# Kernel tuning notes

Hardware: AMD Instinct MI355X
Metric: run time of the kernel (lower is better)

Reference implementation:

```python
import jax, jax.numpy as jnp
import numpy as np

NH, NKVH, HD = 32, 8, 128
SCALE = 0.08838834764831845  # 1/sqrt(128)
SEQ, CTX = 1024, 3072       # new chunk tokens, cached context tokens
NSLOTS = 8192               # e.g. 512 blocks * block_size 16, slot-flattened


def setup_inputs() -> dict:
    key = jax.random.key(0)
    ks = jax.random.split(key, 5)
    q = jax.random.normal(ks[0], (SEQ, NH * HD), dtype=jnp.float32)
    k = jax.random.normal(ks[1], (SEQ, NKVH * HD), dtype=jnp.float32)
    v = jax.random.normal(ks[2], (SEQ, NKVH * HD), dtype=jnp.float32)
    k_cache = jax.random.normal(ks[3], (NSLOTS, NKVH, HD), dtype=jnp.float32)
    v_cache = jax.random.normal(ks[4], (NSLOTS, NKVH, HD), dtype=jnp.float32)
    # new chunk is stored right after the context region
    slot_mapping = jnp.arange(SEQ, dtype=jnp.int32) + CTX
    context_slots = jnp.arange(CTX, dtype=jnp.int32)
    return {"q": q, "k": k, "v": v, "k_cache": k_cache, "v_cache": v_cache,
            "slot_mapping": slot_mapping, "context_slots": context_slots}


def reference(q, k, v, k_cache, v_cache, slot_mapping, context_slots):
    seq = q.shape[0]
    ctx = context_slots.shape[0]
    qh = q.reshape(seq, NH, HD)
    kh = k.reshape(seq, NKVH, HD)
    vh = v.reshape(seq, NKVH, HD)

    # store_kv_cache: scatter new chunk k/v into paged cache slots
    kc = k_cache.at[slot_mapping].set(kh)
    vc = v_cache.at[slot_mapping].set(vh)

    # gather cached context, then chunked-prefill attention over [ctx | chunk]
    k_all = jnp.concatenate([kc[context_slots], kh], axis=0)  # [L, nkvh, hd]
    v_all = jnp.concatenate([vc[context_slots], vh], axis=0)  # [L, nkvh, hd]
    L = ctx + seq

    group = NH // NKVH
    qg = qh.reshape(seq, NKVH, group, HD) * SCALE
    scores = jnp.einsum('qkgd,lkd->kgql', qg, k_all)  # [nkvh, group, seq, L]

    # full visibility of cached context, causal within the new chunk
    mask = jnp.arange(L)[None, :] <= (ctx + jnp.arange(seq))[:, None]  # [seq, L]
    scores = jnp.where(mask[None, None], scores, jnp.finfo(scores.dtype).min)
    p = jax.nn.softmax(scores, axis=-1)

    o = jnp.einsum('kgql,lkd->qkgd', p, v_all)  # [seq, nkvh, group, hd]
    return o.reshape(seq, NH * HD)
```

## Files before the change

kernel.cpp:

```cpp
#include <hip/hip_runtime.h>

#define NH 32
#define NKVH 8
#define HD 128
#define GRP 4
#define SCALE 0.08838834764831845f

typedef __attribute__((ext_vector_type(8))) __bf16 bf16x8;
typedef __attribute__((ext_vector_type(4))) float f32x4;
typedef __attribute__((ext_vector_type(8))) unsigned short ushort8;

__device__ inline unsigned short f2bf(float x) {
  unsigned int u = __float_as_uint(x);
  u += 0x7fffu + ((u >> 16) & 1u);
  return (unsigned short)(u >> 16);
}

__device__ inline float dpp_max16(float x) {
  x = fmaxf(x, __int_as_float(__builtin_amdgcn_mov_dpp(__float_as_int(x), 0xB1, 0xF, 0xF, true)));
  x = fmaxf(x, __int_as_float(__builtin_amdgcn_mov_dpp(__float_as_int(x), 0x4E, 0xF, 0xF, true)));
  x = fmaxf(x, __int_as_float(__builtin_amdgcn_mov_dpp(__float_as_int(x), 0x141, 0xF, 0xF, true)));
  x = fmaxf(x, __int_as_float(__builtin_amdgcn_mov_dpp(__float_as_int(x), 0x140, 0xF, 0xF, true)));
  return x;
}
__device__ inline float dpp_sum16(float x) {
  x += __int_as_float(__builtin_amdgcn_mov_dpp(__float_as_int(x), 0xB1, 0xF, 0xF, true));
  x += __int_as_float(__builtin_amdgcn_mov_dpp(__float_as_int(x), 0x4E, 0xF, 0xF, true));
  x += __int_as_float(__builtin_amdgcn_mov_dpp(__float_as_int(x), 0x141, 0xF, 0xF, true));
  x += __int_as_float(__builtin_amdgcn_mov_dpp(__float_as_int(x), 0x140, 0xF, 0xF, true));
  return x;
}

__device__ inline void load_lds16(const unsigned short* g, unsigned short* l) {
  __builtin_amdgcn_global_load_lds((const __attribute__((address_space(1))) unsigned int*)g,
                                   (__attribute__((address_space(3))) unsigned int*)l, 16, 0, 0);
}

#define PSTR 72

__global__ __launch_bounds__(256) void prepass_kernel(
    const float* __restrict__ k, const float* __restrict__ v,
    const float* __restrict__ kc, const float* __restrict__ vc,
    const int* __restrict__ slots,
    unsigned short* __restrict__ Kws, unsigned short* __restrict__ Vws,
    int ctx, int L, int kblocks)
{
  if (blockIdx.x < (unsigned)kblocks) {
    const int idx = blockIdx.x * 256 + threadIdx.x;
    const int L8  = L * 8;
    const int kvh = idx / L8;
    const int r2  = idx - kvh * L8;
    const int l   = r2 >> 3;
    const int c16 = idx & 7;
    const float* src = (l < ctx)
        ? kc + ((size_t)slots[l] * NKVH + kvh) * HD + c16 * 16
        : k + (size_t)(l - ctx) * (NKVH * HD) + kvh * HD + c16 * 16;
    float4 f[4];
#pragma unroll
    for (int i = 0; i < 4; ++i) f[i] = ((const float4*)src)[i];
    unsigned short* tile = Kws + (size_t)kvh * L * HD + (size_t)(l >> 6) * 8192;
    const int r = l & 63;
    const int c0 = (2 * c16) ^ (r & 7);
    const int c1 = (2 * c16 + 1) ^ (r & 7);
    ushort8 w0, w1;
    w0[0]=f2bf(f[0].x); w0[1]=f2bf(f[0].y); w0[2]=f2bf(f[0].z); w0[3]=f2bf(f[0].w);
    w0[4]=f2bf(f[1].x); w0[5]=f2bf(f[1].y); w0[6]=f2bf(f[1].z); w0[7]=f2bf(f[1].w);
    w1[0]=f2bf(f[2].x); w1[1]=f2bf(f[2].y); w1[2]=f2bf(f[2].z); w1[3]=f2bf(f[2].w);
    w1[4]=f2bf(f[3].x); w1[5]=f2bf(f[3].y); w1[6]=f2bf(f[3].z); w1[7]=f2bf(f[3].w);
    *(ushort8*)&tile[r * 128 + c0 * 8] = w0;
    *(ushort8*)&tile[r * 128 + c1 * 8] = w1;
  } else {
    const int idx = (blockIdx.x - kblocks) * 256 + threadIdx.x;
    const int d   = idx & 127;
    const int t2  = idx >> 7;
    const int L16 = L >> 4;
    const int kvh = t2 / L16;
    const int lc  = t2 - kvh * L16;
    const int l0  = lc * 16;
    unsigned short vals[16];
#pragma unroll
    for (int i = 0; i < 16; ++i) {
      const int l = l0 + i;
      const float* sp = (l < ctx)
          ? vc + ((size_t)slots[l] * NKVH + kvh) * HD + d
          : v + (size_t)(l - ctx) * (NKVH * HD) + kvh * HD + d;
      vals[i] = f2bf(*sp);
    }
    unsigned short* tile = Vws + (size_t)kvh * L * HD + (size_t)(l0 >> 6) * 8192;
    const int lt  = l0 & 63;
    const int cl0 = lt >> 3;
    ushort8 w0, w1;
#pragma unroll
    for (int i = 0; i < 8; ++i) { w0[i] = vals[i]; w1[i] = vals[8 + i]; }
    *(ushort8*)&tile[d * 64 + ((cl0 ^ (d & 7)) * 8)] = w0;
    *(ushort8*)&tile[d * 64 + (((cl0 + 1) ^ (d & 7)) * 8)] = w1;
  }
}

__global__ __launch_bounds__(256, 2) void attn_kernel(
    const float* __restrict__ q,
    const unsigned short* __restrict__ Kws, const unsigned short* __restrict__ Vws,
    float* __restrict__ out, int ctx, int L)
{
  __shared__ __align__(16) unsigned short Ks[2][8192];
  __shared__ __align__(16) unsigned short VTs[2][8192];
  __shared__ __align__(16) unsigned short Ps[4 * 16 * PSTR];

  const int bx   = blockIdx.x;
  const int kvh  = bx & 7;
  const int g    = (bx >> 3) & 3;
  const int qb   = bx >> 5;
  const int q0   = qb * 64;
  const int head = kvh * GRP + g;

  const int tid  = threadIdx.x;
  const int wave = tid >> 6;
  const int lane = tid & 63;
  const int col  = lane & 15;
  const int quad = lane >> 4;

  bf16x8 qf[4];
  {
    const float* qp = q + (size_t)(q0 + wave * 16 + col) * (NH * HD) + head * HD;
#pragma unroll
    for (int kt = 0; kt < 4; ++kt) {
      const float4 a = *(const float4*)(qp + kt * 32 + quad * 8);
      const float4 b = *(const float4*)(qp + kt * 32 + quad * 8 + 4);
      union { ushort8 u; bf16x8 h; } w;
      w.u[0]=f2bf(a.x*SCALE); w.u[1]=f2bf(a.y*SCALE); w.u[2]=f2bf(a.z*SCALE); w.u[3]=f2bf(a.w*SCALE);
      w.u[4]=f2bf(b.x*SCALE); w.u[5]=f2bf(b.y*SCALE); w.u[6]=f2bf(b.z*SCALE); w.u[7]=f2bf(b.w*SCALE);
      qf[kt] = w.h;
    }
  }

  f32x4 accO[8];
#pragma unroll
  for (int i = 0; i < 8; ++i) accO[i] = (f32x4){0.f, 0.f, 0.f, 0.f};
  float mrow[4] = {-1e30f, -1e30f, -1e30f, -1e30f};
  float lrow[4] = {0.f, 0.f, 0.f, 0.f};

  const int rowbase = q0 + wave * 16 + quad * 4;
  const size_t kvbase = (size_t)kvh * L * HD;
  const int n_tiles = (ctx + q0 + 64) >> 6;

  auto dma_tile = [&](int t, int b) {
    const unsigned short* kg = Kws + kvbase + (size_t)t * 8192;
    const unsigned short* vg = Vws + kvbase + (size_t)t * 8192;
#pragma unroll
    for (int j = 0; j < 4; ++j) {
      const int ch = wave * 4 + j;
      load_lds16(kg + ch * 512 + lane * 8, &Ks[b][ch * 512]);
      load_lds16(vg + ch * 512 + lane * 8, &VTs[b][ch * 512]);
    }
  };

  dma_tile(0, 0);

  for (int it = 0; it < n_tiles; ++it) {
    __syncthreads();

    if (it + 1 < n_tiles) dma_tile(it + 1, (it + 1) & 1);

    const unsigned short* Kb = Ks[it & 1];
    const unsigned short* Vb = VTs[it & 1];
    const int kb = it << 6;

    f32x4 S[4];
#pragma unroll
    for (int nt = 0; nt < 4; ++nt) S[nt] = (f32x4){0.f, 0.f, 0.f, 0.f};
#pragma unroll
    for (int kt = 0; kt < 4; ++kt)
#pragma unroll
      for (int nt = 0; nt < 4; ++nt) {
        const int row = nt * 16 + col;
        const bf16x8 kf = *(const bf16x8*)&Kb[row * 128 + (((kt * 4 + quad) ^ (row & 7)) << 3)];
        S[nt] = __builtin_amdgcn_mfma_f32_16x16x32_bf16(qf[kt], kf, S[nt], 0, 0, 0);
      }

    if (kb + 63 > ctx + q0 + wave * 16) {
#pragma unroll
      for (int r = 0; r < 4; ++r) {
        const int bound = ctx + rowbase + r;
#pragma unroll
        for (int nt = 0; nt < 4; ++nt) {
          const int l = kb + nt * 16 + col;
          if (l > bound) S[nt][r] = -1e30f;
        }
      }
    }

    float alpha[4];
#pragma unroll
    for (int r = 0; r < 4; ++r) {
      float mx = fmaxf(fmaxf(S[0][r], S[1][r]), fmaxf(S[2][r], S[3][r]));
      mx = dpp_max16(mx);
      const float mnew = fmaxf(mrow[r], mx);
      alpha[r] = __expf(mrow[r] - mnew);
      float rs = 0.f;
#pragma unroll
      for (int nt = 0; nt < 4; ++nt) {
        const float p = __expf(S[nt][r] - mnew);
        S[nt][r] = p;
        rs += p;
      }
      rs = dpp_sum16(rs);
      lrow[r] = lrow[r] * alpha[r] + rs;
      mrow[r] = mnew;
    }
#pragma unroll
    for (int dd = 0; dd < 8; ++dd)
#pragma unroll
      for (int r = 0; r < 4; ++r)
        accO[dd][r] *= alpha[r];

    unsigned short* pw = &Ps[wave * 16 * PSTR];
#pragma unroll
    for (int nt = 0; nt < 4; ++nt)
#pragma unroll
      for (int r = 0; r < 4; ++r)
        pw[(quad * 4 + r) * PSTR + nt * 16 + col] = f2bf(S[nt][r]);
    asm volatile("s_waitcnt lgkmcnt(0)" ::: "memory");

    bf16x8 pf[2];
    pf[0] = *(const bf16x8*)&pw[col * PSTR + quad * 8];
    pf[1] = *(const bf16x8*)&pw[col * PSTR + 32 + quad * 8];

#pragma unroll
    for (int nt = 0; nt < 8; ++nt)
#pragma unroll
      for (int kt = 0; kt < 2; ++kt) {
        const int d = nt * 16 + col;
        const bf16x8 vf = *(const bf16x8*)&Vb[d * 64 + (((kt * 4 + quad) ^ (d & 7)) << 3)];
        accO[nt] = __builtin_amdgcn_mfma_f32_16x16x32_bf16(pf[kt], vf, accO[nt], 0, 0, 0);
      }
  }

  float inv[4];
#pragma unroll
  for (int r = 0; r < 4; ++r) inv[r] = 1.0f / lrow[r];
  float* op = out + head * HD;
#pragma unroll
  for (int r = 0; r < 4; ++r) {
    float* orow = op + (size_t)(rowbase + r) * (NH * HD);
#pragma unroll
    for (int nt = 0; nt < 8; ++nt)
      orow[nt * 16 + col] = accO[nt][r] * inv[r];
  }
}

extern "C" void kernel_launch(void* const* d_in, const int* in_sizes, int n_in,
                              void* d_out, int out_size, void* d_ws, size_t ws_size,
                              hipStream_t stream) {
  const float* q  = (const float*)d_in[0];
  const float* k  = (const float*)d_in[1];
  const float* v  = (const float*)d_in[2];
  const float* kc = (const float*)d_in[3];
  const float* vc = (const float*)d_in[4];
  const int* ctx_slots = (const int*)d_in[6];
  float* out = (float*)d_out;

  const int seq = in_sizes[0] / (NH * HD);
  const int ctx = in_sizes[6];
  const int L   = ctx + seq;

  unsigned short* Kws = (unsigned short*)d_ws;
  unsigned short* Vws = Kws + (size_t)NKVH * L * HD;

  const int kthreads = NKVH * L * (HD / 16);
  const int vthreads = NKVH * (L / 16) * HD;
  const int kblocks  = kthreads / 256;
  const int vblocks  = vthreads / 256;
  prepass_kernel<<<kblocks + vblocks, 256, 0, stream>>>(k, v, kc, vc, ctx_slots,
                                                        Kws, Vws, ctx, L, kblocks);

  const int nblocks = (seq / 64) * GRP * NKVH;
  attn_kernel<<<nblocks, 256, 0, stream>>>(q, Kws, Vws, out, ctx, L);
}
```

Baseline: 246.4 us.

## Split K/V prepass and give each attention wave two query row tiles

The fused prepass is split into a K conversion kernel and a V kernel that transposes a 64-row tile through shared memory, so global V reads become coalesced float4 loads instead of strided scalar loads. The attention kernel now runs 2 waves per block, each handling 32 query rows. Each K/V fragment read from LDS therefore feeds two MFMAs, halving LDS traffic per FLOP. The cost is higher register pressure and fewer waves per block, which may reduce latency hiding.

```diff
diff --git a/kernel.cpp b/kernel.cpp
--- a/kernel.cpp
+++ b/kernel.cpp
@@ -38,73 +38,79 @@
 
 #define PSTR 72
 
-__global__ __launch_bounds__(256) void prepass_kernel(
-    const float* __restrict__ k, const float* __restrict__ v,
-    const float* __restrict__ kc, const float* __restrict__ vc,
-    const int* __restrict__ slots,
-    unsigned short* __restrict__ Kws, unsigned short* __restrict__ Vws,
-    int ctx, int L, int kblocks)
+__global__ __launch_bounds__(256) void kprep(
+    const float* __restrict__ k, const float* __restrict__ kc,
+    const int* __restrict__ slots, unsigned short* __restrict__ Kws, int ctx, int L)
 {
-  if (blockIdx.x < (unsigned)kblocks) {
-    const int idx = blockIdx.x * 256 + threadIdx.x;
-    const int L8  = L * 8;
-    const int kvh = idx / L8;
-    const int r2  = idx - kvh * L8;
-    const int l   = r2 >> 3;
-    const int c16 = idx & 7;
-    const float* src = (l < ctx)
-        ? kc + ((size_t)slots[l] * NKVH + kvh) * HD + c16 * 16
-        : k + (size_t)(l - ctx) * (NKVH * HD) + kvh * HD + c16 * 16;
-    float4 f[4];
-#pragma unroll
-    for (int i = 0; i < 4; ++i) f[i] = ((const float4*)src)[i];
-    unsigned short* tile = Kws + (size_t)kvh * L * HD + (size_t)(l >> 6) * 8192;
-    const int r = l & 63;
-    const int c0 = (2 * c16) ^ (r & 7);
-    const int c1 = (2 * c16 + 1) ^ (r & 7);
-    ushort8 w0, w1;
-    w0[0]=f2bf(f[0].x); w0[1]=f2bf(f[0].y); w0[2]=f2bf(f[0].z); w0[3]=f2bf(f[0].w);
-    w0[4]=f2bf(f[1].x); w0[5]=f2bf(f[1].y); w0[6]=f2bf(f[1].z); w0[7]=f2bf(f[1].w);
-    w1[0]=f2bf(f[2].x); w1[1]=f2bf(f[2].y); w1[2]=f2bf(f[2].z); w1[3]=f2bf(f[2].w);
-    w1[4]=f2bf(f[3].x); w1[5]=f2bf(f[3].y); w1[6]=f2bf(f[3].z); w1[7]=f2bf(f[3].w);
-    *(ushort8*)&tile[r * 128 + c0 * 8] = w0;
-    *(ushort8*)&tile[r * 128 + c1 * 8] = w1;
-  } else {
-    const int idx = (blockIdx.x - kblocks) * 256 + threadIdx.x;
-    const int d   = idx & 127;
-    const int t2  = idx >> 7;
-    const int L16 = L >> 4;
-    const int kvh = t2 / L16;
-    const int lc  = t2 - kvh * L16;
-    const int l0  = lc * 16;
-    unsigned short vals[16];
-#pragma unroll
-    for (int i = 0; i < 16; ++i) {
-      const int l = l0 + i;
-      const float* sp = (l < ctx)
-          ? vc + ((size_t)slots[l] * NKVH + kvh) * HD + d
-          : v + (size_t)(l - ctx) * (NKVH * HD) + kvh * HD + d;
-      vals[i] = f2bf(*sp);
-    }
-    unsigned short* tile = Vws + (size_t)kvh * L * HD + (size_t)(l0 >> 6) * 8192;
-    const int lt  = l0 & 63;
-    const int cl0 = lt >> 3;
-    ushort8 w0, w1;
-#pragma unroll
-    for (int i = 0; i < 8; ++i) { w0[i] = vals[i]; w1[i] = vals[8 + i]; }
-    *(ushort8*)&tile[d * 64 + ((cl0 ^ (d & 7)) * 8)] = w0;
-    *(ushort8*)&tile[d * 64 + (((cl0 + 1) ^ (d & 7)) * 8)] = w1;
+  const int idx = blockIdx.x * 256 + threadIdx.x;
+  const int L8  = L * 8;
+  const int kvh = idx / L8;
+  const int r2  = idx - kvh * L8;
+  const int l   = r2 >> 3;
+  const int c16 = idx & 7;
+  const float* src = (l < ctx)
+      ? kc + ((size_t)slots[l] * NKVH + kvh) * HD + c16 * 16
+      : k + (size_t)(l - ctx) * (NKVH * HD) + kvh * HD + c16 * 16;
+  float4 f[4];
+#pragma unroll
+  for (int i = 0; i < 4; ++i) f[i] = ((const float4*)src)[i];
+  unsigned short* tile = Kws + (size_t)kvh * L * HD + (size_t)(l >> 6) * 8192;
+  const int r  = l & 63;
+  const int c0 = (2 * c16) ^ (r & 7);
+  const int c1 = (2 * c16 + 1) ^ (r & 7);
+  ushort8 w0, w1;
+  w0[0]=f2bf(f[0].x); w0[1]=f2bf(f[0].y); w0[2]=f2bf(f[0].z); w0[3]=f2bf(f[0].w);
+  w0[4]=f2bf(f[1].x); w0[5]=f2bf(f[1].y); w0[6]=f2bf(f[1].z); w0[7]=f2bf(f[1].w);
+  w1[0]=f2bf(f[2].x); w1[1]=f2bf(f[2].y); w1[2]=f2bf(f[2].z); w1[3]=f2bf(f[2].w);
+  w1[4]=f2bf(f[3].x); w1[5]=f2bf(f[3].y); w1[6]=f2bf(f[3].z); w1[7]=f2bf(f[3].w);
+  *(ushort8*)&tile[r * 128 + c0 * 8] = w0;
+  *(ushort8*)&tile[r * 128 + c1 * 8] = w1;
+}
+
+__global__ __launch_bounds__(256) void vprep(
+    const float* __restrict__ v, const float* __restrict__ vc,
+    const int* __restrict__ slots, unsigned short* __restrict__ Vws,
+    int ctx, int L, int ntiles)
+{
+  __shared__ __align__(16) unsigned short VT[8192];
+  const int t   = blockIdx.x % ntiles;
+  const int kvh = blockIdx.x / ntiles;
+  const int tid = threadIdx.x;
+  const int l   = tid >> 2;
+  const int ds  = tid & 3;
+  const int lg  = t * 64 + l;
+  const float* sp = (lg < ctx)
+      ? vc + ((size_t)slots[lg] * NKVH + kvh) * HD
+      : v + (size_t)(lg - ctx) * (NKVH * HD) + kvh * HD;
+  sp += ds * 32;
+  float4 f[8];
+#pragma unroll
+  for (int i = 0; i < 8; ++i) f[i] = ((const float4*)sp)[i];
+  const int c  = l >> 3;
+  const int lo = l & 7;
+#pragma unroll
+  for (int i = 0; i < 8; ++i) {
+    const int d0 = ds * 32 + i * 4;
+    VT[(d0+0)*64 + ((c ^ ((d0+0)&7)) << 3) + lo] = f2bf(f[i].x);
+    VT[(d0+1)*64 + ((c ^ ((d0+1)&7)) << 3) + lo] = f2bf(f[i].y);
+    VT[(d0+2)*64 + ((c ^ ((d0+2)&7)) << 3) + lo] = f2bf(f[i].z);
+    VT[(d0+3)*64 + ((c ^ ((d0+3)&7)) << 3) + lo] = f2bf(f[i].w);
   }
-}
-
-__global__ __launch_bounds__(256, 2) void attn_kernel(
+  __syncthreads();
+  ushort8* dst = (ushort8*)(Vws + (size_t)kvh * L * HD + (size_t)t * 8192);
+  const ushort8* s8 = (const ushort8*)VT;
+#pragma unroll
+  for (int i = 0; i < 4; ++i) dst[i * 256 + tid] = s8[i * 256 + tid];
+}
+
+__global__ __launch_bounds__(128, 1) void attn_kernel(
     const float* __restrict__ q,
     const unsigned short* __restrict__ Kws, const unsigned short* __restrict__ Vws,
     float* __restrict__ out, int ctx, int L)
 {
   __shared__ __align__(16) unsigned short Ks[2][8192];
   __shared__ __align__(16) unsigned short VTs[2][8192];
-  __shared__ __align__(16) unsigned short Ps[4 * 16 * PSTR];
+  __shared__ __align__(16) unsigned short Ps[2 * 32 * PSTR];
 
   const int bx   = blockIdx.x;
   const int kvh  = bx & 7;
@@ -119,9 +125,10 @@
   const int col  = lane & 15;
   const int quad = lane >> 4;
 
-  bf16x8 qf[4];
-  {
-    const float* qp = q + (size_t)(q0 + wave * 16 + col) * (NH * HD) + head * HD;
+  bf16x8 qf[2][4];
+#pragma unroll
+  for (int mt = 0; mt < 2; ++mt) {
+    const float* qp = q + (size_t)(q0 + wave * 32 + mt * 16 + col) * (NH * HD) + head * HD;
 #pragma unroll
     for (int kt = 0; kt < 4; ++kt) {
       const float4 a = *(const float4*)(qp + kt * 32 + quad * 8);
@@ -129,17 +136,21 @@
       union { ushort8 u; bf16x8 h; } w;
       w.u[0]=f2bf(a.x*SCALE); w.u[1]=f2bf(a.y*SCALE); w.u[2]=f2bf(a.z*SCALE); w.u[3]=f2bf(a.w*SCALE);
       w.u[4]=f2bf(b.x*SCALE); w.u[5]=f2bf(b.y*SCALE); w.u[6]=f2bf(b.z*SCALE); w.u[7]=f2bf(b.w*SCALE);
-      qf[kt] = w.h;
+      qf[mt][kt] = w.h;
     }
   }
 
-  f32x4 accO[8];
-#pragma unroll
-  for (int i = 0; i < 8; ++i) accO[i] = (f32x4){0.f, 0.f, 0.f, 0.f};
-  float mrow[4] = {-1e30f, -1e30f, -1e30f, -1e30f};
-  float lrow[4] = {0.f, 0.f, 0.f, 0.f};
-
-  const int rowbase = q0 + wave * 16 + quad * 4;
+  f32x4 accO[2][8];
+#pragma unroll
+  for (int mt = 0; mt < 2; ++mt)
+#pragma unroll
+    for (int i = 0; i < 8; ++i) accO[mt][i] = (f32x4){0.f, 0.f, 0.f, 0.f};
+  float mrow[2][4], lrow[2][4];
+#pragma unroll
+  for (int mt = 0; mt < 2; ++mt)
+#pragma unroll
+    for (int r = 0; r < 4; ++r) { mrow[mt][r] = -1e30f; lrow[mt][r] = 0.f; }
+
   const size_t kvbase = (size_t)kvh * L * HD;
   const int n_tiles = (ctx + q0 + 64) >> 6;
 
@@ -147,8 +158,8 @@
     const unsigned short* kg = Kws + kvbase + (size_t)t * 8192;
     const unsigned short* vg = Vws + kvbase + (size_t)t * 8192;
 #pragma unroll
-    for (int j = 0; j < 4; ++j) {
-      const int ch = wave * 4 + j;
+    for (int j = 0; j < 8; ++j) {
+      const int ch = wave * 8 + j;
       load_lds16(kg + ch * 512 + lane * 8, &Ks[b][ch * 512]);
       load_lds16(vg + ch * 512 + lane * 8, &VTs[b][ch * 512]);
     }
@@ -165,65 +176,80 @@
     const unsigned short* Vb = VTs[it & 1];
     const int kb = it << 6;
 
-    f32x4 S[4];
-#pragma unroll
-    for (int nt = 0; nt < 4; ++nt) S[nt] = (f32x4){0.f, 0.f, 0.f, 0.f};
+    f32x4 S[2][4];
+#pragma unroll
+    for (int mt = 0; mt < 2; ++mt)
+#pragma unroll
+      for (int nt = 0; nt < 4; ++nt) S[mt][nt] = (f32x4){0.f, 0.f, 0.f, 0.f};
 #pragma unroll
     for (int kt = 0; kt < 4; ++kt)
 #pragma unroll
       for (int nt = 0; nt < 4; ++nt) {
         const int row = nt * 16 + col;
         const bf16x8 kf = *(const bf16x8*)&Kb[row * 128 + (((kt * 4 + quad) ^ (row & 7)) << 3)];
-        S[nt] = __builtin_amdgcn_mfma_f32_16x16x32_bf16(qf[kt], kf, S[nt], 0, 0, 0);
+        S[0][nt] = __builtin_amdgcn_mfma_f32_16x16x32_bf16(qf[0][kt], kf, S[0][nt], 0, 0, 0);
+        S[1][nt] = __builtin_amdgcn_mfma_f32_16x16x32_bf16(qf[1][kt], kf, S[1][nt], 0, 0, 0);
       }
 
-    if (kb + 63 > ctx + q0 + wave * 16) {
-#pragma unroll
-      for (int r = 0; r < 4; ++r) {
-        const int bound = ctx + rowbase + r;
-#pragma unroll
-        for (int nt = 0; nt < 4; ++nt) {
-          const int l = kb + nt * 16 + col;
-          if (l > bound) S[nt][r] = -1e30f;
+    if (kb + 63 > ctx + q0 + wave * 32) {
+#pragma unroll
+      for (int mt = 0; mt < 2; ++mt) {
+        const int rb = q0 + wave * 32 + mt * 16 + quad * 4;
+#pragma unroll
+        for (int r = 0; r < 4; ++r) {
+          const int bound = ctx + rb + r;
+#pragma unroll
+          for (int nt = 0; nt < 4; ++nt) {
+            const int l = kb + nt * 16 + col;
+            if (l > bound) S[mt][nt][r] = -1e30f;
+          }
         }
       }
     }
 
-    float alpha[4];
-#pragma unroll
-    for (int r = 0; r < 4; ++r) {
-      float mx = fmaxf(fmaxf(S[0][r], S[1][r]), fmaxf(S[2][r], S[3][r]));
-      mx = dpp_max16(mx);
-      const float mnew = fmaxf(mrow[r], mx);
-      alpha[r] = __expf(mrow[r] - mnew);
-      float rs = 0.f;
-#pragma unroll
-      for (int nt = 0; nt < 4; ++nt) {
-        const float p = __expf(S[nt][r] - mnew);
-        S[nt][r] = p;
-        rs += p;
+#pragma unroll
+    for (int mt = 0; mt < 2; ++mt) {
+      float alpha[4];
+#pragma unroll
+      for (int r = 0; r < 4; ++r) {
+        float mx = fmaxf(fmaxf(S[mt][0][r], S[mt][1][r]), fmaxf(S[mt][2][r], S[mt][3][r]));
+        mx = dpp_max16(mx);
+        const float mnew = fmaxf(mrow[mt][r], mx);
+        alpha[r] = __expf(mrow[mt][r] - mnew);
+        float rs = 0.f;
+#pragma unroll
+        for (int nt = 0; nt < 4; ++nt) {
+          const float p = __expf(S[mt][nt][r] - mnew);
+          S[mt][nt][r] = p;
+          rs += p;
+        }
+        rs = dpp_sum16(rs);
+        lrow[mt][r] = lrow[mt][r] * alpha[r] + rs;
+        mrow[mt][r] = mnew;
       }
-      rs = dpp_sum16(rs);
-      lrow[r] = lrow[r] * alpha[r] + rs;
-      mrow[r] = mnew;
-    }
-#pragma unroll
-    for (int dd = 0; dd < 8; ++dd)
-#pragma unroll
-      for (int r = 0; r < 4; ++r)
-        accO[dd][r] *= alpha[r];
-
-    unsigned short* pw = &Ps[wave * 16 * PSTR];
-#pragma unroll
-    for (int nt = 0; nt < 4; ++nt)
-#pragma unroll
-      for (int r = 0; r < 4; ++r)
-        pw[(quad * 4 + r) * PSTR + nt * 16 + col] = f2bf(S[nt][r]);
+#pragma unroll
+      for (int dd = 0; dd < 8; ++dd)
+#pragma unroll
+        for (int r = 0; r < 4; ++r)
+          accO[mt][dd][r] *= alpha[r];
+    }
+
+    unsigned short* pw = &Ps[wave * 32 * PSTR];
+#pragma unroll
+    for (int mt = 0; mt < 2; ++mt)
+#pragma unroll
+      for (int nt = 0; nt < 4; ++nt)
+#pragma unroll
+        for (int r = 0; r < 4; ++r)
+          pw[(mt * 16 + quad * 4 + r) * PSTR + nt * 16 + col] = f2bf(S[mt][nt][r]);
     asm volatile("s_waitcnt lgkmcnt(0)" ::: "memory");
 
-    bf16x8 pf[2];
-    pf[0] = *(const bf16x8*)&pw[col * PSTR + quad * 8];
-    pf[1] = *(const bf16x8*)&pw[col * PSTR + 32 + quad * 8];
+    bf16x8 pf[2][2];
+#pragma unroll
+    for (int mt = 0; mt < 2; ++mt) {
+      pf[mt][0] = *(const bf16x8*)&pw[(mt * 16 + col) * PSTR + quad * 8];
+      pf[mt][1] = *(const bf16x8*)&pw[(mt * 16 + col) * PSTR + 32 + quad * 8];
+    }
 
 #pragma unroll
     for (int nt = 0; nt < 8; ++nt)
@@ -231,20 +257,22 @@
       for (int kt = 0; kt < 2; ++kt) {
         const int d = nt * 16 + col;
         const bf16x8 vf = *(const bf16x8*)&Vb[d * 64 + (((kt * 4 + quad) ^ (d & 7)) << 3)];
-        accO[nt] = __builtin_amdgcn_mfma_f32_16x16x32_bf16(pf[kt], vf, accO[nt], 0, 0, 0);
+        accO[0][nt] = __builtin_amdgcn_mfma_f32_16x16x32_bf16(pf[0][kt], vf, accO[0][nt], 0, 0, 0);
+        accO[1][nt] = __builtin_amdgcn_mfma_f32_16x16x32_bf16(pf[1][kt], vf, accO[1][nt], 0, 0, 0);
       }
   }
 
-  float inv[4];
-#pragma unroll
-  for (int r = 0; r < 4; ++r) inv[r] = 1.0f / lrow[r];
-  float* op = out + head * HD;
-#pragma unroll
-  for (int r = 0; r < 4; ++r) {
-    float* orow = op + (size_t)(rowbase + r) * (NH * HD);
-#pragma unroll
-    for (int nt = 0; nt < 8; ++nt)
-      orow[nt * 16 + col] = accO[nt][r] * inv[r];
+#pragma unroll
+  for (int mt = 0; mt < 2; ++mt) {
+    const int rb = q0 + wave * 32 + mt * 16 + quad * 4;
+#pragma unroll
+    for (int r = 0; r < 4; ++r) {
+      const float inv = 1.0f / lrow[mt][r];
+      float* orow = out + (size_t)(rb + r) * (NH * HD) + head * HD;
+#pragma unroll
+      for (int nt = 0; nt < 8; ++nt)
+        orow[nt * 16 + col] = accO[mt][nt][r] * inv;
+    }
   }
 }
 
@@ -262,17 +290,14 @@
   const int seq = in_sizes[0] / (NH * HD);
   const int ctx = in_sizes[6];
   const int L   = ctx + seq;
+  const int ntiles = L >> 6;
 
   unsigned short* Kws = (unsigned short*)d_ws;
   unsigned short* Vws = Kws + (size_t)NKVH * L * HD;
 
-  const int kthreads = NKVH * L * (HD / 16);
-  const int vthreads = NKVH * (L / 16) * HD;
-  const int kblocks  = kthreads / 256;
-  const int vblocks  = vthreads / 256;
-  prepass_kernel<<<kblocks + vblocks, 256, 0, stream>>>(k, v, kc, vc, ctx_slots,
-                                                        Kws, Vws, ctx, L, kblocks);
+  kprep<<<(NKVH * L * 8) / 256, 256, 0, stream>>>(k, kc, ctx_slots, Kws, ctx, L);
+  vprep<<<NKVH * ntiles, 256, 0, stream>>>(v, vc, ctx_slots, Vws, ctx, L, ntiles);
 
   const int nblocks = (seq / 64) * GRP * NKVH;
-  attn_kernel<<<nblocks, 256, 0, stream>>>(q, Kws, Vws, out, ctx, L);
-}
+  attn_kernel<<<nblocks, 128, 0, stream>>>(q, Kws, Vws, out, ctx, L);
+}
```

Measured after the change: 300.5 us. 1.22x slower.
